# Kernel tuning notes

Measured on AMD Instinct MI355X. Metric: run time of the kernel, lower is better.

The kernel has to match this reference:

```python
import jax, jax.numpy as jnp
import numpy as np

N_HEAD, D_MODEL, D_HEAD = 16, 1024, 64
BSZ, SEQLEN = 2, 2048
ROPE_BASE = 10000.0


def _rope_tables(seqlen, d_head, base=ROPE_BASE):
    # freqs_cis = exp(i * t * theta_j), theta_j = base^(-2j/d_head)
    inv_freq = 1.0 / (base ** (np.arange(0, d_head, 2, dtype=np.float32) / d_head))
    t = np.arange(seqlen, dtype=np.float32)
    ang = np.outer(t, inv_freq)  # [S, d_head//2]
    return jnp.asarray(np.cos(ang)), jnp.asarray(np.sin(ang))


def setup_inputs() -> dict:
    key = jax.random.key(0)
    ks = jax.random.split(key, 5)
    x = jax.random.normal(ks[0], (BSZ, SEQLEN, D_MODEL), dtype=jnp.float32)
    freqs_cos, freqs_sin = _rope_tables(SEQLEN, D_HEAD)
    scale = 0.02
    # weights stored as (in, out) so projection is x @ w
    wq = jax.random.normal(ks[1], (D_MODEL, N_HEAD * D_HEAD), dtype=jnp.float32) * scale
    wk = jax.random.normal(ks[2], (D_MODEL, N_HEAD * D_HEAD), dtype=jnp.float32) * scale
    wv = jax.random.normal(ks[3], (D_MODEL, N_HEAD * D_HEAD), dtype=jnp.float32) * scale
    wo = jax.random.normal(ks[4], (N_HEAD * D_HEAD, D_MODEL), dtype=jnp.float32) * scale
    return {"x": x, "freqs_cos": freqs_cos, "freqs_sin": freqs_sin,
            "wq": wq, "wk": wk, "wv": wv, "wo": wo}


def _apply_rope(t, cos, sin):
    # t: [B, S, H, Dh]; complex pairs are consecutive elements (x0 + i*x1)
    B, S, H, Dh = t.shape
    tf = t.astype(jnp.float32).reshape(B, S, H, Dh // 2, 2)
    t0, t1 = tf[..., 0], tf[..., 1]
    c = cos[None, :, None, :]  # [1, S, 1, Dh//2]
    s = sin[None, :, None, :]
    o0 = t0 * c - t1 * s
    o1 = t0 * s + t1 * c
    return jnp.stack([o0, o1], axis=-1).reshape(B, S, H, Dh).astype(t.dtype)


def reference(x, freqs_cos, freqs_sin, wq, wk, wv, wo):
    B, S, _ = x.shape
    H, Dh = N_HEAD, D_HEAD
    q = jnp.einsum('bsd,de->bse', x, wq).reshape(B, S, H, Dh)
    k = jnp.einsum('bsd,de->bse', x, wk).reshape(B, S, H, Dh)
    v = jnp.einsum('bsd,de->bse', x, wv).reshape(B, S, H, Dh)
    q = _apply_rope(q, freqs_cos, freqs_sin)
    k = _apply_rope(k, freqs_cos, freqs_sin)
    # [B, H, S, Dh]
    q = q.transpose(0, 2, 1, 3)
    k = k.transpose(0, 2, 1, 3)
    v = v.transpose(0, 2, 1, 3)
    scores = jnp.einsum('bhqd,bhkd->bhqk', q, k) / jnp.sqrt(jnp.float32(Dh))
    probs = jax.nn.softmax(scores.astype(jnp.float32), axis=-1).astype(q.dtype)
    out = jnp.einsum('bhqk,bhkd->bhqd', probs, v)  # [B, H, S, Dh]
    out = out.transpose(0, 2, 1, 3).reshape(B, S, H * Dh)
    return jnp.einsum('bse,ed->bsd', out, wo)
```

## Files before the change

### kernel.cpp

```cpp
#include <hip/hip_runtime.h>
#include <math.h>

#define BSZ 2
#define SEQ 2048
#define NH 16
#define DH 64
#define DM 1024
#define HD 1024

typedef _Float16 h16;
typedef _Float16 half8 __attribute__((ext_vector_type(8)));
typedef _Float16 half4 __attribute__((ext_vector_type(4)));
typedef float f32x4 __attribute__((ext_vector_type(4)));

__device__ __forceinline__ f32x4 mfma16(half8 a, half8 b, f32x4 c) {
    return __builtin_amdgcn_mfma_f32_16x16x32_f16(a, b, c, 0, 0, 0);
}

__device__ __forceinline__ void async_copy16(h16* lds, const h16* g) {
    __builtin_amdgcn_global_load_lds(
        (const __attribute__((address_space(1))) unsigned int*)g,
        (__attribute__((address_space(3))) unsigned int*)lds, 16, 0, 0);
}

#define SWZ(cb, r) ((((cb) ^ ((r) & 7)) * 8))

__global__ __launch_bounds__(256) void cvt_x_kernel(const float* __restrict__ x,
                                                    h16* __restrict__ x16)
{
    int i = (blockIdx.x * 256 + threadIdx.x) * 8;
    float4 a = *(const float4*)&x[i];
    float4 b = *(const float4*)&x[i + 4];
    half8 o;
    o[0] = (h16)a.x; o[1] = (h16)a.y; o[2] = (h16)a.z; o[3] = (h16)a.w;
    o[4] = (h16)b.x; o[5] = (h16)b.y; o[6] = (h16)b.z; o[7] = (h16)b.w;
    *(half8*)&x16[i] = o;
}

__global__ __launch_bounds__(256) void wtrans_kernel(
    const float* __restrict__ wq, const float* __restrict__ wk,
    const float* __restrict__ wv, const float* __restrict__ wo,
    h16* __restrict__ wt)
{
    const float* w = (blockIdx.z == 0) ? wq : (blockIdx.z == 1) ? wk
                   : (blockIdx.z == 2) ? wv : wo;
    h16* ot = wt + (size_t)blockIdx.z * DM * DM;
    __shared__ float tile[64][68];
    const int k0 = blockIdx.y * 64, n0 = blockIdx.x * 64;
    const int t = threadIdx.x;
    const int r = t >> 2, c4 = (t & 3) * 16;
#pragma unroll
    for (int i = 0; i < 16; i += 4) {
        float4 v = *(const float4*)&w[(size_t)(k0 + r) * DM + n0 + c4 + i];
        tile[r][c4 + i + 0] = v.x; tile[r][c4 + i + 1] = v.y;
        tile[r][c4 + i + 2] = v.z; tile[r][c4 + i + 3] = v.w;
    }
    __syncthreads();
#pragma unroll
    for (int g = 0; g < 2; ++g) {
        half8 hh;
#pragma unroll
        for (int j = 0; j < 8; ++j)
            hh[j] = (h16)tile[c4 + g * 8 + j][r];
        *(half8*)&ot[(size_t)(n0 + r) * DM + k0 + c4 + g * 8] = hh;
    }
}

__global__ __launch_bounds__(512, 4) void qkv_kernel(
    const h16* __restrict__ x16, const h16* __restrict__ wt,
    const float* __restrict__ fcos, const float* __restrict__ fsin,
    h16* __restrict__ Q16, h16* __restrict__ K16, h16* __restrict__ VT16)
{
    const int z = blockIdx.z;
    const h16* __restrict__ bw = wt + (size_t)z * DM * DM;

    __shared__ h16 smem[17408];
    h16* As = smem;
    h16* Bs = smem + 8192;
    h16* Vt = smem;

    const int m0 = blockIdx.y * 128;
    const int n0 = blockIdx.x * 128;
    const int t  = threadIdx.x;
    const int w  = t >> 6, ln = t & 63;
    const int L  = ln & 15, U = ln >> 4;
    const int wm = (w & 3) * 32;
    const int wn = (w >> 2) * 64;

    const int sr  = ln >> 3;
    const int scb = (ln & 7) ^ sr;

    f32x4 acc[2][4];
#pragma unroll
    for (int i = 0; i < 2; ++i)
#pragma unroll
        for (int j = 0; j < 4; ++j) acc[i][j] = (f32x4)0.0f;

    for (int k0 = 0; k0 < DM; k0 += 64) {
        __syncthreads();
#pragma unroll
        for (int c = 0; c < 2; ++c) {
            int rb = w * 16 + c * 8;
            async_copy16(&As[rb * 64], &x16[(size_t)(m0 + rb + sr) * DM + k0 + scb * 8]);
            async_copy16(&Bs[rb * 64], &bw [(size_t)(n0 + rb + sr) * DM + k0 + scb * 8]);
        }
        __syncthreads();

#pragma unroll
        for (int ks = 0; ks < 2; ++ks) {
            half8 af[2], bf[4];
#pragma unroll
            for (int mt = 0; mt < 2; ++mt)
                af[mt] = *(const half8*)&As[(wm + mt * 16 + L) * 64 + SWZ(ks * 4 + U, L)];
#pragma unroll
            for (int nt = 0; nt < 4; ++nt)
                bf[nt] = *(const half8*)&Bs[(wn + nt * 16 + L) * 64 + SWZ(ks * 4 + U, L)];
#pragma unroll
            for (int mt = 0; mt < 2; ++mt)
#pragma unroll
                for (int nt = 0; nt < 4; ++nt)
                    acc[mt][nt] = mfma16(bf[nt], af[mt], acc[mt][nt]);
        }
    }

    const int b = m0 >> 11;
    const int sbase = m0 & 2047;

    if (z < 2) {
        const float sc = (z == 0) ? 0.125f * 1.44269504088896f : 1.0f;
#pragma unroll
        for (int mt = 0; mt < 2; ++mt) {
            int s = sbase + wm + mt * 16 + L;
            const float* ct = &fcos[s * 32];
            const float* st = &fsin[s * 32];
#pragma unroll
            for (int nt = 0; nt < 4; ++nt) {
                int nl = n0 + wn + nt * 16 + U * 4;
                int d = nl & 63, h = nl >> 6;
                int pd = d >> 1;
                float cv0 = ct[pd], sv0 = st[pd];
                float cv1 = ct[pd + 1], sv1 = st[pd + 1];
                float v0 = acc[mt][nt][0], v1 = acc[mt][nt][1];
                float v2 = acc[mt][nt][2], v3 = acc[mt][nt][3];
                float o0 = (v0 * cv0 - v1 * sv0) * sc;
                float o1 = (v0 * sv0 + v1 * cv0) * sc;
                float o2 = (v2 * cv1 - v3 * sv1) * sc;
                float o3 = (v2 * sv1 + v3 * cv1) * sc;
                size_t addr = ((size_t)(b * NH + h) * SEQ + s) * DH + d;
                half4 kk;
                kk[0] = (h16)o0; kk[1] = (h16)o1; kk[2] = (h16)o2; kk[3] = (h16)o3;
                if (z == 0) *(half4*)&Q16[addr] = kk;
                else        *(half4*)&K16[addr] = kk;
            }
        }
    } else {
        __syncthreads();
#pragma unroll
        for (int mt = 0; mt < 2; ++mt)
#pragma unroll
            for (int nt = 0; nt < 4; ++nt)
#pragma unroll
                for (int r = 0; r < 4; ++r) {
                    int nloc = wn + nt * 16 + U * 4 + r;
                    int sloc = wm + mt * 16 + L;
                    Vt[nloc * 136 + sloc] = (h16)acc[mt][nt][r];
                }
        __syncthreads();
#pragma unroll
        for (int i = 0; i < 4; ++i) {
            int c = i * 512 + t;
            int dl = c >> 4;
            int s8 = (c & 15) * 8;
            half8 vv = *(const half8*)&Vt[dl * 136 + s8];
            int n = n0 + dl;
            int d = n & 63, h = n >> 6;
            *(half8*)&VT16[((size_t)(b * NH + h) * DH + d) * SEQ + sbase + s8] = vv;
        }
    }
}

#define PLD 136

__global__ __launch_bounds__(512, 4) void attn_kernel(
    const h16* __restrict__ Q16, const h16* __restrict__ K16,
    const h16* __restrict__ VT16, h16* __restrict__ A16)
{
    __shared__ h16 Ks[128 * 64];
    __shared__ h16 VTs[64 * 128];
    __shared__ __align__(16) h16 Ps[128 * PLD];
    __shared__ float mlbuf[8][2][16][2];

    float* Obuf = (float*)Ps;

    const int t = threadIdx.x, w = t >> 6, ln = t & 63;
    const int L = ln & 15, U = ln >> 4;
    const int pair = w >> 1, half = w & 1;
    const int qw = pair * 32, kh = half * 64;
    const int q0 = blockIdx.x * 128;
    const int bh = blockIdx.y;
    const size_t base = (size_t)bh * SEQ * DH;

    half8 qf[2][2];
#pragma unroll
    for (int qb = 0; qb < 2; ++qb)
#pragma unroll
        for (int ks = 0; ks < 2; ++ks)
            qf[qb][ks] = *(const half8*)&Q16[base + (size_t)(q0 + qw + qb * 16 + L) * DH + ks * 32 + U * 8];

    f32x4 O[4][2];
#pragma unroll
    for (int dt = 0; dt < 4; ++dt)
#pragma unroll
        for (int qb = 0; qb < 2; ++qb) O[dt][qb] = (f32x4)0.0f;
    float m_i[2] = {-1e30f, -1e30f}, l_i[2] = {0.0f, 0.0f};

    const int sr  = ln >> 3;
    const int scb = (ln & 7) ^ sr;

    for (int j0 = 0; j0 < SEQ; j0 += 128) {
        __syncthreads();
#pragma unroll
        for (int c = 0; c < 2; ++c) {
            int rbk = c * 64 + w * 8;
            async_copy16(&Ks[rbk * 64], &K16[base + (size_t)(j0 + rbk + sr) * DH + scb * 8]);
        }
#pragma unroll
        for (int c = 0; c < 2; ++c) {
            int rv = (w * 2 + c) * 4;
            int c16 = (ln & 15) ^ ((rv + U) & 15);
            async_copy16(&VTs[rv * 128], &VT16[base + (size_t)(rv + U) * SEQ + j0 + c16 * 8]);
        }
        __syncthreads();

        f32x4 S[4][2];
#pragma unroll
        for (int nt = 0; nt < 4; ++nt) {
            S[nt][0] = (f32x4)0.0f;
            S[nt][1] = (f32x4)0.0f;
#pragma unroll
            for (int ks = 0; ks < 2; ++ks) {
                half8 kf = *(const half8*)&Ks[(kh + nt * 16 + L) * 64 + SWZ(ks * 4 + U, L)];
                S[nt][0] = mfma16(kf, qf[0][ks], S[nt][0]);
                S[nt][1] = mfma16(kf, qf[1][ks], S[nt][1]);
            }
        }

#pragma unroll
        for (int qb = 0; qb < 2; ++qb) {
            float mx = -1e30f;
#pragma unroll
            for (int nt = 0; nt < 4; ++nt)
#pragma unroll
                for (int r = 0; r < 4; ++r) mx = fmaxf(mx, S[nt][qb][r]);
            mx = fmaxf(mx, __shfl_xor(mx, 16, 64));
            mx = fmaxf(mx, __shfl_xor(mx, 32, 64));
            float mnew  = fmaxf(m_i[qb], mx);
            float alpha = exp2f(m_i[qb] - mnew);
            float rs = 0.0f;
            int prow = (qw + qb * 16 + L) * PLD + kh;
#pragma unroll
            for (int nt = 0; nt < 4; ++nt) {
                float p0 = exp2f(S[nt][qb][0] - mnew);
                float p1 = exp2f(S[nt][qb][1] - mnew);
                float p2 = exp2f(S[nt][qb][2] - mnew);
                float p3 = exp2f(S[nt][qb][3] - mnew);
                rs += (p0 + p1) + (p2 + p3);
                half4 pq;
                pq[0] = (h16)p0; pq[1] = (h16)p1; pq[2] = (h16)p2; pq[3] = (h16)p3;
                *(half4*)&Ps[prow + nt * 16 + U * 4] = pq;
            }
            rs += __shfl_xor(rs, 16, 64);
            rs += __shfl_xor(rs, 32, 64);
            m_i[qb] = mnew;
            l_i[qb] = l_i[qb] * alpha + rs;
#pragma unroll
            for (int dt = 0; dt < 4; ++dt) O[dt][qb] *= alpha;
        }

        half8 pf[2][2];
#pragma unroll
        for (int qb = 0; qb < 2; ++qb)
#pragma unroll
            for (int ks2 = 0; ks2 < 2; ++ks2)
                pf[qb][ks2] = *(const half8*)&Ps[(qw + qb * 16 + L) * PLD + kh + ks2 * 32 + U * 8];
#pragma unroll
        for (int dt = 0; dt < 4; ++dt)
#pragma unroll
            for (int ks2 = 0; ks2 < 2; ++ks2) {
                half8 vf = *(const half8*)&VTs[(dt * 16 + L) * 128 + ((half * 8 + ks2 * 4 + U) ^ L) * 8];
                O[dt][0] = mfma16(vf, pf[0][ks2], O[dt][0]);
                O[dt][1] = mfma16(vf, pf[1][ks2], O[dt][1]);
            }
    }

    if (U == 0) {
        mlbuf[w][0][L][0] = m_i[0]; mlbuf[w][0][L][1] = l_i[0];
        mlbuf[w][1][L][0] = m_i[1]; mlbuf[w][1][L][1] = l_i[1];
    }
    __syncthreads();
    const int pw = w ^ 1;
    float l_tot[2];
#pragma unroll
    for (int qb = 0; qb < 2; ++qb) {
        float mp = mlbuf[pw][qb][L][0], lp = mlbuf[pw][qb][L][1];
        float m  = fmaxf(m_i[qb], mp);
        float ss = exp2f(m_i[qb] - m);
        float sp = exp2f(mp - m);
        l_tot[qb] = l_i[qb] * ss + lp * sp;
#pragma unroll
        for (int dt = 0; dt < 4; ++dt) O[dt][qb] *= ss;
    }
    if (half) {
#pragma unroll
        for (int qb = 0; qb < 2; ++qb)
#pragma unroll
            for (int dt = 0; dt < 4; ++dt)
                *(f32x4*)&Obuf[(qw + qb * 16 + L) * 68 + dt * 16 + U * 4] = O[dt][qb];
    }
    __syncthreads();
    if (!half) {
        const int b = bh >> 4, hh = bh & 15;
#pragma unroll
        for (int qb = 0; qb < 2; ++qb) {
            float inv = 1.0f / l_tot[qb];
            int s = q0 + qw + qb * 16 + L;
#pragma unroll
            for (int dt = 0; dt < 4; ++dt) {
                f32x4 op = *(const f32x4*)&Obuf[(qw + qb * 16 + L) * 68 + dt * 16 + U * 4];
                half4 o4;
#pragma unroll
                for (int r = 0; r < 4; ++r)
                    o4[r] = (h16)((O[dt][qb][r] + op[r]) * inv);
                *(half4*)&A16[(size_t)(b * SEQ + s) * HD + hh * DH + dt * 16 + U * 4] = o4;
            }
        }
    }
}

__global__ __launch_bounds__(512, 4) void oproj_kernel(
    const h16* __restrict__ A16, const h16* __restrict__ bw,
    float* __restrict__ out)
{
    __shared__ h16 As[128 * 64];
    __shared__ h16 Bs[64 * 64];

    const int m0 = blockIdx.y * 128;
    const int n0 = blockIdx.x * 64;
    const int t  = threadIdx.x;
    const int w  = t >> 6, ln = t & 63;
    const int L  = ln & 15, U = ln >> 4;

    const int sr  = ln >> 3;
    const int scb = (ln & 7) ^ sr;

    f32x4 acc[4];
#pragma unroll
    for (int j = 0; j < 4; ++j) acc[j] = (f32x4)0.0f;

    for (int k0 = 0; k0 < DM; k0 += 64) {
        __syncthreads();
#pragma unroll
        for (int c = 0; c < 2; ++c) {
            int rb = w * 16 + c * 8;
            async_copy16(&As[rb * 64], &A16[(size_t)(m0 + rb + sr) * DM + k0 + scb * 8]);
        }
        {
            int rb = w * 8;
            async_copy16(&Bs[rb * 64], &bw[(size_t)(n0 + rb + sr) * DM + k0 + scb * 8]);
        }
        __syncthreads();

#pragma unroll
        for (int ks = 0; ks < 2; ++ks) {
            half8 af, bf[4];
            af = *(const half8*)&As[(w * 16 + L) * 64 + SWZ(ks * 4 + U, L)];
#pragma unroll
            for (int nt = 0; nt < 4; ++nt)
                bf[nt] = *(const half8*)&Bs[(nt * 16 + L) * 64 + SWZ(ks * 4 + U, L)];
#pragma unroll
            for (int nt = 0; nt < 4; ++nt)
                acc[nt] = mfma16(af, bf[nt], acc[nt]);
        }
    }

#pragma unroll
    for (int nt = 0; nt < 4; ++nt)
#pragma unroll
        for (int r = 0; r < 4; ++r) {
            int row = m0 + w * 16 + U * 4 + r;
            int col = n0 + nt * 16 + L;
            out[(size_t)row * DM + col] = acc[nt][r];
        }
}

extern "C" void kernel_launch(void* const* d_in, const int* in_sizes, int n_in,
                              void* d_out, int out_size, void* d_ws, size_t ws_size,
                              hipStream_t stream)
{
    const float* x    = (const float*)d_in[0];
    const float* fcos = (const float*)d_in[1];
    const float* fsin = (const float*)d_in[2];
    const float* wq   = (const float*)d_in[3];
    const float* wk   = (const float*)d_in[4];
    const float* wv   = (const float*)d_in[5];
    const float* wo   = (const float*)d_in[6];
    float* out = (float*)d_out;

    const size_t M4 = (size_t)4 * 1024 * 1024;
    h16* x16  = (h16*)d_ws;
    h16* wt   = x16 + M4;
    h16* Q16  = wt + M4;
    h16* K16  = Q16 + M4;
    h16* VT16 = K16 + M4;
    h16* A16  = VT16 + M4;

    cvt_x_kernel<<<2048, 256, 0, stream>>>(x, x16);
    wtrans_kernel<<<dim3(16, 16, 4), 256, 0, stream>>>(wq, wk, wv, wo, wt);
    qkv_kernel<<<dim3(8, 32, 3), 512, 0, stream>>>(x16, wt, fcos, fsin,
                                                   Q16, K16, VT16);
    attn_kernel<<<dim3(16, 32), 512, 0, stream>>>(Q16, K16, VT16, A16);
    oproj_kernel<<<dim3(16, 32), 512, 0, stream>>>(A16, wt + 3 * (size_t)DM * DM, out);
}
```

Before: 218.0 us.

## Merge prep kernels and enlarge QKV and output-projection GEMM tiles

The x conversion and weight transpose kernels become one prep launch, with the x conversion handled by extra z-slices. The QKV GEMM tile grows from 128x128 to 256x128, so each warp computes 64x64. The output projection tile grows from 128x64 to 128x128. Larger tiles raise operand reuse and cut global loads per FLOP, but they use more registers and LDS and halve the block count, which may lower occupancy and wave fill on the GPU.

```diff
diff --git a/kernel.cpp b/kernel.cpp
--- a/kernel.cpp
+++ b/kernel.cpp
@@ -25,29 +25,32 @@
 
 #define SWZ(cb, r) ((((cb) ^ ((r) & 7)) * 8))
 
-__global__ __launch_bounds__(256) void cvt_x_kernel(const float* __restrict__ x,
-                                                    h16* __restrict__ x16)
+__global__ __launch_bounds__(256) void prep_kernel(
+    const float* __restrict__ x, const float* __restrict__ wq,
+    const float* __restrict__ wk, const float* __restrict__ wv,
+    const float* __restrict__ wo,
+    h16* __restrict__ x16, h16* __restrict__ wt)
 {
-    int i = (blockIdx.x * 256 + threadIdx.x) * 8;
-    float4 a = *(const float4*)&x[i];
-    float4 b = *(const float4*)&x[i + 4];
-    half8 o;
-    o[0] = (h16)a.x; o[1] = (h16)a.y; o[2] = (h16)a.z; o[3] = (h16)a.w;
-    o[4] = (h16)b.x; o[5] = (h16)b.y; o[6] = (h16)b.z; o[7] = (h16)b.w;
-    *(half8*)&x16[i] = o;
-}
-
-__global__ __launch_bounds__(256) void wtrans_kernel(
-    const float* __restrict__ wq, const float* __restrict__ wk,
-    const float* __restrict__ wv, const float* __restrict__ wo,
-    h16* __restrict__ wt)
-{
-    const float* w = (blockIdx.z == 0) ? wq : (blockIdx.z == 1) ? wk
-                   : (blockIdx.z == 2) ? wv : wo;
-    h16* ot = wt + (size_t)blockIdx.z * DM * DM;
+    const int z = blockIdx.z;
+    const int t = threadIdx.x;
+    if (z == 4) {
+        int flat = blockIdx.y * 16 + blockIdx.x;
+#pragma unroll
+        for (int i = 0; i < 8; ++i) {
+            int idx = flat * 16384 + i * 2048 + t * 8;
+            float4 a = *(const float4*)&x[idx];
+            float4 b = *(const float4*)&x[idx + 4];
+            half8 o;
+            o[0] = (h16)a.x; o[1] = (h16)a.y; o[2] = (h16)a.z; o[3] = (h16)a.w;
+            o[4] = (h16)b.x; o[5] = (h16)b.y; o[6] = (h16)b.z; o[7] = (h16)b.w;
+            *(half8*)&x16[idx] = o;
+        }
+        return;
+    }
+    const float* w = (z == 0) ? wq : (z == 1) ? wk : (z == 2) ? wv : wo;
+    h16* ot = wt + (size_t)z * DM * DM;
     __shared__ float tile[64][68];
     const int k0 = blockIdx.y * 64, n0 = blockIdx.x * 64;
-    const int t = threadIdx.x;
     const int r = t >> 2, c4 = (t & 3) * 16;
 #pragma unroll
     for (int i = 0; i < 16; i += 4) {
@@ -74,49 +77,53 @@
     const int z = blockIdx.z;
     const h16* __restrict__ bw = wt + (size_t)z * DM * DM;
 
-    __shared__ h16 smem[17408];
+    __shared__ h16 smem[24576];
     h16* As = smem;
-    h16* Bs = smem + 8192;
+    h16* Bs = smem + 16384;
     h16* Vt = smem;
 
-    const int m0 = blockIdx.y * 128;
+    const int m0 = blockIdx.y * 256;
     const int n0 = blockIdx.x * 128;
     const int t  = threadIdx.x;
     const int w  = t >> 6, ln = t & 63;
     const int L  = ln & 15, U = ln >> 4;
-    const int wm = (w & 3) * 32;
+    const int wm = (w & 3) * 64;
     const int wn = (w >> 2) * 64;
 
     const int sr  = ln >> 3;
     const int scb = (ln & 7) ^ sr;
 
-    f32x4 acc[2][4];
-#pragma unroll
-    for (int i = 0; i < 2; ++i)
+    f32x4 acc[4][4];
+#pragma unroll
+    for (int i = 0; i < 4; ++i)
 #pragma unroll
         for (int j = 0; j < 4; ++j) acc[i][j] = (f32x4)0.0f;
 
     for (int k0 = 0; k0 < DM; k0 += 64) {
         __syncthreads();
+#pragma unroll
+        for (int c = 0; c < 4; ++c) {
+            int rb = w * 32 + c * 8;
+            async_copy16(&As[rb * 64], &x16[(size_t)(m0 + rb + sr) * DM + k0 + scb * 8]);
+        }
 #pragma unroll
         for (int c = 0; c < 2; ++c) {
             int rb = w * 16 + c * 8;
-            async_copy16(&As[rb * 64], &x16[(size_t)(m0 + rb + sr) * DM + k0 + scb * 8]);
-            async_copy16(&Bs[rb * 64], &bw [(size_t)(n0 + rb + sr) * DM + k0 + scb * 8]);
+            async_copy16(&Bs[rb * 64], &bw[(size_t)(n0 + rb + sr) * DM + k0 + scb * 8]);
         }
         __syncthreads();
 
 #pragma unroll
         for (int ks = 0; ks < 2; ++ks) {
-            half8 af[2], bf[4];
-#pragma unroll
-            for (int mt = 0; mt < 2; ++mt)
+            half8 af[4], bf[4];
+#pragma unroll
+            for (int mt = 0; mt < 4; ++mt)
                 af[mt] = *(const half8*)&As[(wm + mt * 16 + L) * 64 + SWZ(ks * 4 + U, L)];
 #pragma unroll
             for (int nt = 0; nt < 4; ++nt)
                 bf[nt] = *(const half8*)&Bs[(wn + nt * 16 + L) * 64 + SWZ(ks * 4 + U, L)];
 #pragma unroll
-            for (int mt = 0; mt < 2; ++mt)
+            for (int mt = 0; mt < 4; ++mt)
 #pragma unroll
                 for (int nt = 0; nt < 4; ++nt)
                     acc[mt][nt] = mfma16(bf[nt], af[mt], acc[mt][nt]);
@@ -129,7 +136,7 @@
     if (z < 2) {
         const float sc = (z == 0) ? 0.125f * 1.44269504088896f : 1.0f;
 #pragma unroll
-        for (int mt = 0; mt < 2; ++mt) {
+        for (int mt = 0; mt < 4; ++mt) {
             int s = sbase + wm + mt * 16 + L;
             const float* ct = &fcos[s * 32];
             const float* st = &fsin[s * 32];
@@ -154,27 +161,32 @@
             }
         }
     } else {
-        __syncthreads();
-#pragma unroll
-        for (int mt = 0; mt < 2; ++mt)
-#pragma unroll
-            for (int nt = 0; nt < 4; ++nt)
-#pragma unroll
-                for (int r = 0; r < 4; ++r) {
-                    int nloc = wn + nt * 16 + U * 4 + r;
-                    int sloc = wm + mt * 16 + L;
-                    Vt[nloc * 136 + sloc] = (h16)acc[mt][nt][r];
-                }
-        __syncthreads();
-#pragma unroll
-        for (int i = 0; i < 4; ++i) {
-            int c = i * 512 + t;
-            int dl = c >> 4;
-            int s8 = (c & 15) * 8;
-            half8 vv = *(const half8*)&Vt[dl * 136 + s8];
-            int n = n0 + dl;
-            int d = n & 63, h = n >> 6;
-            *(half8*)&VT16[((size_t)(b * NH + h) * DH + d) * SEQ + sbase + s8] = vv;
+#pragma unroll
+        for (int h2 = 0; h2 < 2; ++h2) {
+            __syncthreads();
+            if ((wm >> 7) == h2) {
+#pragma unroll
+                for (int mt = 0; mt < 4; ++mt)
+#pragma unroll
+                    for (int nt = 0; nt < 4; ++nt)
+#pragma unroll
+                        for (int r = 0; r < 4; ++r) {
+                            int nloc = wn + nt * 16 + U * 4 + r;
+                            int sloc = (wm & 127) + mt * 16 + L;
+                            Vt[nloc * 136 + sloc] = (h16)acc[mt][nt][r];
+                        }
+            }
+            __syncthreads();
+#pragma unroll
+            for (int i = 0; i < 4; ++i) {
+                int c = i * 512 + t;
+                int dl = c >> 4;
+                int s8 = (c & 15) * 8;
+                half8 vv = *(const half8*)&Vt[dl * 136 + s8];
+                int n = n0 + dl;
+                int d = n & 63, h = n >> 6;
+                *(half8*)&VT16[((size_t)(b * NH + h) * DH + d) * SEQ + sbase + h2 * 128 + s8] = vv;
+            }
         }
     }
 }
@@ -342,20 +354,24 @@
     float* __restrict__ out)
 {
     __shared__ h16 As[128 * 64];
-    __shared__ h16 Bs[64 * 64];
+    __shared__ h16 Bs[128 * 64];
 
     const int m0 = blockIdx.y * 128;
-    const int n0 = blockIdx.x * 64;
+    const int n0 = blockIdx.x * 128;
     const int t  = threadIdx.x;
     const int w  = t >> 6, ln = t & 63;
     const int L  = ln & 15, U = ln >> 4;
+    const int wm = (w & 3) * 32;
+    const int wn = (w >> 2) * 64;
 
     const int sr  = ln >> 3;
     const int scb = (ln & 7) ^ sr;
 
-    f32x4 acc[4];
-#pragma unroll
-    for (int j = 0; j < 4; ++j) acc[j] = (f32x4)0.0f;
+    f32x4 acc[2][4];
+#pragma unroll
+    for (int i = 0; i < 2; ++i)
+#pragma unroll
+        for (int j = 0; j < 4; ++j) acc[i][j] = (f32x4)0.0f;
 
     for (int k0 = 0; k0 < DM; k0 += 64) {
         __syncthreads();
@@ -363,34 +379,37 @@
         for (int c = 0; c < 2; ++c) {
             int rb = w * 16 + c * 8;
             async_copy16(&As[rb * 64], &A16[(size_t)(m0 + rb + sr) * DM + k0 + scb * 8]);
-        }
-        {
-            int rb = w * 8;
-            async_copy16(&Bs[rb * 64], &bw[(size_t)(n0 + rb + sr) * DM + k0 + scb * 8]);
+            async_copy16(&Bs[rb * 64], &bw [(size_t)(n0 + rb + sr) * DM + k0 + scb * 8]);
         }
         __syncthreads();
 
 #pragma unroll
         for (int ks = 0; ks < 2; ++ks) {
-            half8 af, bf[4];
-            af = *(const half8*)&As[(w * 16 + L) * 64 + SWZ(ks * 4 + U, L)];
+            half8 af[2], bf[4];
+#pragma unroll
+            for (int mt = 0; mt < 2; ++mt)
+                af[mt] = *(const half8*)&As[(wm + mt * 16 + L) * 64 + SWZ(ks * 4 + U, L)];
 #pragma unroll
             for (int nt = 0; nt < 4; ++nt)
-                bf[nt] = *(const half8*)&Bs[(nt * 16 + L) * 64 + SWZ(ks * 4 + U, L)];
-#pragma unroll
-            for (int nt = 0; nt < 4; ++nt)
-                acc[nt] = mfma16(af, bf[nt], acc[nt]);
-        }
-    }
-
-#pragma unroll
-    for (int nt = 0; nt < 4; ++nt)
-#pragma unroll
-        for (int r = 0; r < 4; ++r) {
-            int row = m0 + w * 16 + U * 4 + r;
-            int col = n0 + nt * 16 + L;
-            out[(size_t)row * DM + col] = acc[nt][r];
-        }
+                bf[nt] = *(const half8*)&Bs[(wn + nt * 16 + L) * 64 + SWZ(ks * 4 + U, L)];
+#pragma unroll
+            for (int mt = 0; mt < 2; ++mt)
+#pragma unroll
+                for (int nt = 0; nt < 4; ++nt)
+                    acc[mt][nt] = mfma16(af[mt], bf[nt], acc[mt][nt]);
+        }
+    }
+
+#pragma unroll
+    for (int mt = 0; mt < 2; ++mt)
+#pragma unroll
+        for (int nt = 0; nt < 4; ++nt)
+#pragma unroll
+            for (int r = 0; r < 4; ++r) {
+                int row = m0 + wm + mt * 16 + U * 4 + r;
+                int col = n0 + wn + nt * 16 + L;
+                out[(size_t)row * DM + col] = acc[mt][nt][r];
+            }
 }
 
 extern "C" void kernel_launch(void* const* d_in, const int* in_sizes, int n_in,
@@ -414,10 +433,9 @@
     h16* VT16 = K16 + M4;
     h16* A16  = VT16 + M4;
 
-    cvt_x_kernel<<<2048, 256, 0, stream>>>(x, x16);
-    wtrans_kernel<<<dim3(16, 16, 4), 256, 0, stream>>>(wq, wk, wv, wo, wt);
-    qkv_kernel<<<dim3(8, 32, 3), 512, 0, stream>>>(x16, wt, fcos, fsin,
+    prep_kernel<<<dim3(16, 16, 5), 256, 0, stream>>>(x, wq, wk, wv, wo, x16, wt);
+    qkv_kernel<<<dim3(8, 16, 3), 512, 0, stream>>>(x16, wt, fcos, fsin,
                                                    Q16, K16, VT16);
     attn_kernel<<<dim3(16, 32), 512, 0, stream>>>(Q16, K16, VT16, A16);
-    oproj_kernel<<<dim3(16, 32), 512, 0, stream>>>(A16, wt + 3 * (size_t)DM * DM, out);
-}
+    oproj_kernel<<<dim3(8, 32), 512, 0, stream>>>(A16, wt + 3 * (size_t)DM * DM, out);
+}
```

Result: slower. 227.6 us (+4.4%).
